# Performance work log

Hardware: AMD Instinct MI355X
Metric: run time of the kernel (lower is better)

Reference implementation:

```python
import jax, jax.numpy as jnp
import numpy as np

N_QUBITS = 4
N_LAYERS = 3
BATCH = 1048576  # 2**20; batched state vector [B, 2,2,2,2] complex64 = 128 MB


def setup_inputs() -> dict:
    key = jax.random.key(0)
    k1, k2 = jax.random.split(key)
    x = jax.random.normal(k1, (BATCH, N_QUBITS), dtype=jnp.float32)
    q_weights = jax.random.normal(k2, (N_LAYERS, N_QUBITS, 3), dtype=jnp.float32) * 0.1
    return {"x": x, "q_weights": q_weights}


def _ry_mat(theta):
    # RY(t) = [[cos t/2, -sin t/2], [sin t/2, cos t/2]]; theta: [] or [B]
    c = jnp.cos(theta * 0.5).astype(jnp.complex64)
    s = jnp.sin(theta * 0.5).astype(jnp.complex64)
    return jnp.stack([jnp.stack([c, -s], -1), jnp.stack([s, c], -1)], -2)


def _rz_mat(theta):
    # RZ(t) = diag(e^{-it/2}, e^{it/2})
    e = jnp.exp(-0.5j * theta.astype(jnp.complex64))
    z = jnp.zeros_like(e)
    return jnp.stack([jnp.stack([e, z], -1), jnp.stack([z, jnp.conj(e)], -1)], -2)


def _apply_1q(state, U, wire):
    # state: [B,2,2,2,2]; U: [2,2] (shared) or [B,2,2] (per-sample)
    ax = wire + 1
    state = jnp.moveaxis(state, ax, -1)
    if U.ndim == 3:
        state = jnp.einsum('b...o,bno->b...n', state, U)
    else:
        state = jnp.einsum('b...o,no->b...n', state, U)
    return jnp.moveaxis(state, -1, ax)


def _cnot(state, c, t):
    # flip target bit on the control=1 slice
    ca, ta = c + 1, t + 1
    s0 = jnp.take(state, 0, axis=ca)
    s1 = jnp.take(state, 1, axis=ca)
    ta2 = ta if ta < ca else ta - 1
    s1 = jnp.flip(s1, axis=ta2)
    return jnp.stack([s0, s1], axis=ca)


def _circuit(x, q_weights):
    B = x.shape[0]
    xn = jnp.tanh(x) * jnp.pi  # [B, 4]
    # |0000>
    state = jnp.zeros((B,) + (2,) * N_QUBITS, dtype=jnp.complex64)
    state = state.at[:, 0, 0, 0, 0].set(1.0 + 0.0j)
    # angle encoding: RY(2x_i) then RZ(x_i), per-sample batched 2x2 gates
    for i in range(N_QUBITS):
        state = _apply_1q(state, _ry_mat(2.0 * xn[:, i]), i)
        state = _apply_1q(state, _rz_mat(xn[:, i]), i)
    # variational layers: Rot(phi,theta,omega) = RZ(omega) @ RY(theta) @ RZ(phi)
    for l in range(N_LAYERS):
        for i in range(N_QUBITS):
            phi, theta, omega = q_weights[l, i, 0], q_weights[l, i, 1], q_weights[l, i, 2]
            U = _rz_mat(omega) @ _ry_mat(theta) @ _rz_mat(phi)
            state = _apply_1q(state, U, i)
        for i in range(N_QUBITS):
            state = _cnot(state, i, (i + 1) % N_QUBITS)
    # <Z_i> = p(bit_i=0) - p(bit_i=1)
    probs = jnp.abs(state) ** 2  # [B,2,2,2,2] real
    evs = []
    for i in range(N_QUBITS):
        axes = tuple(a for a in range(1, N_QUBITS + 1) if a != i + 1)
        marg = jnp.sum(probs, axis=axes)  # [B, 2]
        evs.append(marg[:, 0] - marg[:, 1])
    return jnp.stack(evs, axis=-1).astype(jnp.float32)  # [B, 4]


def reference(x, q_weights):
    return _circuit(x, q_weights)
```

## Files before the change

kernel.cpp:

```cpp
#include <hip/hip_runtime.h>


struct C { float r, i; };

__device__ __forceinline__ C cmul(C a, C b) {
    C o;
    o.r = fmaf(a.r, b.r, -(a.i * b.i));
    o.i = fmaf(a.r, b.i,   a.i * b.r);
    return o;
}

__device__ __forceinline__ C cmadd(float ur, float ui, float wr, float wi, C a, C b) {
    C o;
    o.r = fmaf(ur, a.r, fmaf(-ui, a.i, fmaf(wr, b.r, -(wi * b.i))));
    o.i = fmaf(ur, a.i, fmaf( ui, a.r, fmaf(wr, b.i,   wi * b.r)));
    return o;
}

template <int BP>
__device__ __forceinline__ void apply_gate(C st[16], float4 A4, float4 B4) {
#pragma unroll
    for (int i = 0; i < 8; i++) {
        const int lo = ((i >> BP) << (BP + 1)) | (i & ((1 << BP) - 1));
        const int hi = lo | (1 << BP);
        const C a = st[lo], b = st[hi];
        st[lo] = cmadd(A4.x, A4.y, A4.z, A4.w, a, b);
        st[hi] = cmadd(B4.x, B4.y, B4.z, B4.w, a, b);
    }
}

template <int CB, int TB>
__device__ __forceinline__ void cnot(C st[16]) {
#pragma unroll
    for (int i = 0; i < 16; i++) {
        if ((i & (1 << CB)) && !(i & (1 << TB))) {
            C t = st[i];
            st[i] = st[i | (1 << TB)];
            st[i | (1 << TB)] = t;
        }
    }
}

struct Enc { float r0, i0, r1, i1; };
__device__ __forceinline__ Enc encode(float xq) {
    const float ax = fabsf(xq);
    const float e  = __builtin_amdgcn_exp2f(ax * -2.8853900817779268f);
    const float r  = __builtin_amdgcn_rcpf(1.0f + e);
    const float t  = copysignf((1.0f - e) * r, xq);
    const float sh = __builtin_amdgcn_sinf(t * 0.25f);
    const float ch = __builtin_amdgcn_cosf(t * 0.25f);
    const float s  = 2.0f * sh * ch;
    const float c  = fmaf(-2.0f * sh, sh, 1.0f);
    return {c * ch, -(c * sh), s * ch, s * sh};
}

__global__ __launch_bounds__(256, 6) void qlayer_kernel(const float* __restrict__ x,
                                                        const float* __restrict__ qw,
                                                        float* __restrict__ out, int B) {
    __shared__ float4 Ug[12][2];
    const int tid = threadIdx.x;
    if (tid < 12) {
        const float phi = qw[tid * 3 + 0];
        const float th  = qw[tid * 3 + 1];
        const float om  = qw[tid * 3 + 2];
        float s, c;   __sincosf(0.5f * th, &s, &c);
        float sa, ca; __sincosf(0.5f * (phi + om), &sa, &ca);
        float sb, cb; __sincosf(0.5f * (phi - om), &sb, &cb);
        Ug[tid][0] = make_float4(c * ca, -c * sa, -s * cb, -s * sb);
        Ug[tid][1] = make_float4(s * cb, -s * sb, c * ca, c * sa);
    }
    __syncthreads();

    const int b = blockIdx.x * 256 + tid;
    if (b >= B) return;

    const float4 xv = reinterpret_cast<const float4*>(x)[b];
    const float xs[4] = {xv.x, xv.y, xv.z, xv.w};

    C v[4][2];
#pragma unroll
    for (int q = 0; q < 4; q++) {
        const Enc e = encode(xs[q]);
        const C a{e.r0, e.i0}, bv{e.r1, e.i1};
        const float4 A4 = Ug[q][0], B4 = Ug[q][1];
        v[q][0] = cmadd(A4.x, A4.y, A4.z, A4.w, a, bv);
        v[q][1] = cmadd(B4.x, B4.y, B4.z, B4.w, a, bv);
    }

    C t01[4], t23[4];
#pragma unroll
    for (int i = 0; i < 4; i++) {
        t01[i] = cmul(v[0][(i >> 1) & 1], v[1][i & 1]);
        t23[i] = cmul(v[2][(i >> 1) & 1], v[3][i & 1]);
    }
    C st[16];
#pragma unroll
    for (int i = 0; i < 16; i++) st[i] = cmul(t01[i >> 2], t23[i & 3]);

    cnot<3, 2>(st); cnot<2, 1>(st); cnot<1, 0>(st); cnot<0, 3>(st);

    apply_gate<3>(st, Ug[4][0], Ug[4][1]);
    apply_gate<2>(st, Ug[5][0], Ug[5][1]);
    apply_gate<1>(st, Ug[6][0], Ug[6][1]);
    apply_gate<0>(st, Ug[7][0], Ug[7][1]);
    cnot<3, 2>(st); cnot<2, 1>(st); cnot<1, 0>(st); cnot<0, 3>(st);
    apply_gate<3>(st, Ug[8][0], Ug[8][1]);
    apply_gate<2>(st, Ug[9][0], Ug[9][1]);
    apply_gate<1>(st, Ug[10][0], Ug[10][1]);
    apply_gate<0>(st, Ug[11][0], Ug[11][1]);
    cnot<3, 2>(st); cnot<2, 1>(st); cnot<1, 0>(st); cnot<0, 3>(st);

    float s0 = 0.f, s1 = 0.f, s2 = 0.f, s3 = 0.f;
#pragma unroll
    for (int i = 0; i < 16; i++) {
        const float p = fmaf(st[i].r, st[i].r, st[i].i * st[i].i);
        if (i & 8) s3 += p;
        if (i & 4) s2 += p;
        if (i & 2) s1 += p;
        if (i & 1) s0 += p;
    }

    float4 ev;
    ev.x = fmaf(-2.0f, s3, 1.0f);
    ev.y = fmaf(-2.0f, s2, 1.0f);
    ev.z = fmaf(-2.0f, s1, 1.0f);
    ev.w = fmaf(-2.0f, s0, 1.0f);
    reinterpret_cast<float4*>(out)[b] = ev;
}

extern "C" void kernel_launch(void* const* d_in, const int* in_sizes, int n_in,
                              void* d_out, int out_size, void* d_ws, size_t ws_size,
                              hipStream_t stream) {
    const float* x  = (const float*)d_in[0];
    const float* qw = (const float*)d_in[1];
    float* out = (float*)d_out;
    const int B = in_sizes[0] / 4;
    const int blocks = (B + 255) / 256;
    qlayer_kernel<<<blocks, 256, 0, stream>>>(x, qw, out, B);
}
```

Measured before the change: 97.63 us.

## Precompose variational circuit into 16x16 unitary and apply via split-f16 MFMA

A tiny precompute kernel builds the fixed 16x16 complex unitary of all CNOT and variational layers (layers 1-2) from the weights. It stores it as hi/lo f16 real-embedded 32x32 matrices in workspace. The main kernel writes each sample's state through LDS as split f16 and applies the unitary with three MFMA 16x16x32 products to keep near-fp32 accuracy. This replaces per-thread scalar gate arithmetic with matrix-core work, at the cost of an extra launch, heavy LDS traffic, two block barriers and lower occupancy.

```diff
diff --git a/kernel.cpp b/kernel.cpp
--- a/kernel.cpp
+++ b/kernel.cpp
@@ -1,5 +1,8 @@
 #include <hip/hip_runtime.h>
 
+
+using f16x8 = __attribute__((ext_vector_type(8))) _Float16;
+using f32x4 = __attribute__((ext_vector_type(4))) float;
 
 struct C { float r, i; };
 
@@ -54,9 +57,10 @@
     return {c * ch, -(c * sh), s * ch, s * sh};
 }
 
-__global__ __launch_bounds__(256, 6) void qlayer_kernel(const float* __restrict__ x,
-                                                        const float* __restrict__ qw,
-                                                        float* __restrict__ out, int B) {
+#define WS_WLO 2048
+#define WS_UG0 4096
+
+__global__ void qcompose_kernel(const float* __restrict__ qw, float* __restrict__ ws) {
     __shared__ float4 Ug[12][2];
     const int tid = threadIdx.x;
     if (tid < 12) {
@@ -71,10 +75,74 @@
     }
     __syncthreads();
 
-    const int b = blockIdx.x * 256 + tid;
-    if (b >= B) return;
-
-    const float4 xv = reinterpret_cast<const float4*>(x)[b];
+    if (tid < 4) {
+        float4* o = reinterpret_cast<float4*>(reinterpret_cast<char*>(ws) + WS_UG0);
+        o[2 * tid]     = Ug[tid][0];
+        o[2 * tid + 1] = Ug[tid][1];
+    }
+
+    if (tid < 16) {
+        C st[16];
+#pragma unroll
+        for (int i = 0; i < 16; i++) { st[i].r = 0.0f; st[i].i = 0.0f; }
+        st[tid].r = 1.0f;
+
+        cnot<3, 2>(st); cnot<2, 1>(st); cnot<1, 0>(st); cnot<0, 3>(st);
+        apply_gate<3>(st, Ug[4][0], Ug[4][1]);
+        apply_gate<2>(st, Ug[5][0], Ug[5][1]);
+        apply_gate<1>(st, Ug[6][0], Ug[6][1]);
+        apply_gate<0>(st, Ug[7][0], Ug[7][1]);
+        cnot<3, 2>(st); cnot<2, 1>(st); cnot<1, 0>(st); cnot<0, 3>(st);
+        apply_gate<3>(st, Ug[8][0], Ug[8][1]);
+        apply_gate<2>(st, Ug[9][0], Ug[9][1]);
+        apply_gate<1>(st, Ug[10][0], Ug[10][1]);
+        apply_gate<0>(st, Ug[11][0], Ug[11][1]);
+        cnot<3, 2>(st); cnot<2, 1>(st); cnot<1, 0>(st); cnot<0, 3>(st);
+
+        _Float16* whi = reinterpret_cast<_Float16*>(ws);
+        _Float16* wlo = reinterpret_cast<_Float16*>(reinterpret_cast<char*>(ws) + WS_WLO);
+        const int k0 = 2 * tid, k1 = k0 + 1;
+#pragma unroll
+        for (int d = 0; d < 16; d++) {
+            const int j0 = 2 * d, j1 = j0 + 1;
+            const float vr = st[d].r, vi = st[d].i;
+            float v[4]  = {vr, vi, -vi, vr};
+            int   jj[4] = {j0, j1, j0, j1};
+            int   kk[4] = {k0, k0, k1, k1};
+#pragma unroll
+            for (int e = 0; e < 4; e++) {
+                _Float16 h = (_Float16)v[e];
+                _Float16 l = (_Float16)((v[e] - (float)h) * 2048.0f);
+                whi[jj[e] * 32 + kk[e]] = h;
+                wlo[jj[e] * 32 + kk[e]] = l;
+            }
+        }
+    }
+}
+
+__global__ __launch_bounds__(256, 4) void qlayer_kernel(const float* __restrict__ x,
+                                                        const float* __restrict__ ws,
+                                                        float* __restrict__ out, int B) {
+    __shared__ __align__(16) unsigned char lds[4 * 64 * 144];
+    const int tid  = threadIdx.x;
+    const int lane = tid & 63;
+    const int wid  = tid >> 6;
+    char* slab  = reinterpret_cast<char*>(lds) + wid * (64 * 144);
+    char* myrow = slab + lane * 144;
+
+    const char* wsb = reinterpret_cast<const char*>(ws);
+
+    const int jrow = lane & 15;
+    const int kb   = (lane >> 4) * 16;
+    const f16x8 Bh0 = *reinterpret_cast<const f16x8*>(wsb + jrow * 64 + kb);
+    const f16x8 Bh1 = *reinterpret_cast<const f16x8*>(wsb + (jrow + 16) * 64 + kb);
+    const f16x8 Bl0 = *reinterpret_cast<const f16x8*>(wsb + WS_WLO + jrow * 64 + kb);
+    const f16x8 Bl1 = *reinterpret_cast<const f16x8*>(wsb + WS_WLO + (jrow + 16) * 64 + kb);
+    const float4* ug0 = reinterpret_cast<const float4*>(wsb + WS_UG0);
+
+    const int b  = blockIdx.x * 256 + tid;
+    const int bl = (b < B) ? b : (B - 1);
+    const float4 xv = reinterpret_cast<const float4*>(x)[bl];
     const float xs[4] = {xv.x, xv.y, xv.z, xv.w};
 
     C v[4][2];
@@ -82,7 +150,7 @@
     for (int q = 0; q < 4; q++) {
         const Enc e = encode(xs[q]);
         const C a{e.r0, e.i0}, bv{e.r1, e.i1};
-        const float4 A4 = Ug[q][0], B4 = Ug[q][1];
+        const float4 A4 = ug0[2 * q], B4 = ug0[2 * q + 1];
         v[q][0] = cmadd(A4.x, A4.y, A4.z, A4.w, a, bv);
         v[q][1] = cmadd(B4.x, B4.y, B4.z, B4.w, a, bv);
     }
@@ -97,35 +165,75 @@
 #pragma unroll
     for (int i = 0; i < 16; i++) st[i] = cmul(t01[i >> 2], t23[i & 3]);
 
-    cnot<3, 2>(st); cnot<2, 1>(st); cnot<1, 0>(st); cnot<0, 3>(st);
-
-    apply_gate<3>(st, Ug[4][0], Ug[4][1]);
-    apply_gate<2>(st, Ug[5][0], Ug[5][1]);
-    apply_gate<1>(st, Ug[6][0], Ug[6][1]);
-    apply_gate<0>(st, Ug[7][0], Ug[7][1]);
-    cnot<3, 2>(st); cnot<2, 1>(st); cnot<1, 0>(st); cnot<0, 3>(st);
-    apply_gate<3>(st, Ug[8][0], Ug[8][1]);
-    apply_gate<2>(st, Ug[9][0], Ug[9][1]);
-    apply_gate<1>(st, Ug[10][0], Ug[10][1]);
-    apply_gate<0>(st, Ug[11][0], Ug[11][1]);
-    cnot<3, 2>(st); cnot<2, 1>(st); cnot<1, 0>(st); cnot<0, 3>(st);
+#pragma unroll
+    for (int c = 0; c < 4; c++) {
+        f16x8 vh, vl;
+#pragma unroll
+        for (int d = 0; d < 4; d++) {
+            const float fr = st[4 * c + d].r, fi = st[4 * c + d].i;
+            const _Float16 hr = (_Float16)fr, hi_ = (_Float16)fi;
+            vh[2 * d]     = hr;
+            vh[2 * d + 1] = hi_;
+            vl[2 * d]     = (_Float16)((fr - (float)hr) * 2048.0f);
+            vl[2 * d + 1] = (_Float16)((fi - (float)hi_) * 2048.0f);
+        }
+        *reinterpret_cast<f16x8*>(myrow + c * 16)      = vh;
+        *reinterpret_cast<f16x8*>(myrow + 64 + c * 16) = vl;
+    }
+
+    __syncthreads();
+
+    const f32x4 Z = {0.f, 0.f, 0.f, 0.f};
+#pragma unroll
+    for (int m = 0; m < 4; m++) {
+        const char* arow = slab + (16 * m + (lane & 15)) * 144 + kb;
+        const f16x8 Ah = *reinterpret_cast<const f16x8*>(arow);
+        const f16x8 Al = *reinterpret_cast<const f16x8*>(arow + 64);
+
+        f32x4 main0 = __builtin_amdgcn_mfma_f32_16x16x32_f16(Ah, Bh0, Z, 0, 0, 0);
+        f32x4 corr0 = __builtin_amdgcn_mfma_f32_16x16x32_f16(Ah, Bl0, Z, 0, 0, 0);
+        corr0       = __builtin_amdgcn_mfma_f32_16x16x32_f16(Al, Bh0, corr0, 0, 0, 0);
+        f32x4 main1 = __builtin_amdgcn_mfma_f32_16x16x32_f16(Ah, Bh1, Z, 0, 0, 0);
+        f32x4 corr1 = __builtin_amdgcn_mfma_f32_16x16x32_f16(Ah, Bl1, Z, 0, 0, 0);
+        corr1       = __builtin_amdgcn_mfma_f32_16x16x32_f16(Al, Bh1, corr1, 0, 0, 0);
+
+        const int srow = 16 * m + 4 * (lane >> 4);
+        const int col  = lane & 15;
+#pragma unroll
+        for (int r = 0; r < 4; r++) {
+            float* crow = reinterpret_cast<float*>(slab + (srow + r) * 144);
+            crow[col]      = fmaf(corr0[r], 4.8828125e-4f, main0[r]);
+            crow[16 + col] = fmaf(corr1[r], 4.8828125e-4f, main1[r]);
+        }
+    }
+
+    __syncthreads();
+
+    float cv[32];
+#pragma unroll
+    for (int c = 0; c < 8; c++) {
+        const float4 q4 = *reinterpret_cast<const float4*>(myrow + c * 16);
+        cv[4 * c] = q4.x; cv[4 * c + 1] = q4.y; cv[4 * c + 2] = q4.z; cv[4 * c + 3] = q4.w;
+    }
 
     float s0 = 0.f, s1 = 0.f, s2 = 0.f, s3 = 0.f;
 #pragma unroll
-    for (int i = 0; i < 16; i++) {
-        const float p = fmaf(st[i].r, st[i].r, st[i].i * st[i].i);
-        if (i & 8) s3 += p;
-        if (i & 4) s2 += p;
-        if (i & 2) s1 += p;
-        if (i & 1) s0 += p;
-    }
-
-    float4 ev;
-    ev.x = fmaf(-2.0f, s3, 1.0f);
-    ev.y = fmaf(-2.0f, s2, 1.0f);
-    ev.z = fmaf(-2.0f, s1, 1.0f);
-    ev.w = fmaf(-2.0f, s0, 1.0f);
-    reinterpret_cast<float4*>(out)[b] = ev;
+    for (int d = 0; d < 16; d++) {
+        const float p = fmaf(cv[2 * d], cv[2 * d], cv[2 * d + 1] * cv[2 * d + 1]);
+        if (d & 8) s3 += p;
+        if (d & 4) s2 += p;
+        if (d & 2) s1 += p;
+        if (d & 1) s0 += p;
+    }
+
+    if (b < B) {
+        float4 ev;
+        ev.x = fmaf(-2.0f, s3, 1.0f);
+        ev.y = fmaf(-2.0f, s2, 1.0f);
+        ev.z = fmaf(-2.0f, s1, 1.0f);
+        ev.w = fmaf(-2.0f, s0, 1.0f);
+        reinterpret_cast<float4*>(out)[b] = ev;
+    }
 }
 
 extern "C" void kernel_launch(void* const* d_in, const int* in_sizes, int n_in,
@@ -134,7 +242,9 @@
     const float* x  = (const float*)d_in[0];
     const float* qw = (const float*)d_in[1];
     float* out = (float*)d_out;
+    float* ws  = (float*)d_ws;
     const int B = in_sizes[0] / 4;
     const int blocks = (B + 255) / 256;
-    qlayer_kernel<<<blocks, 256, 0, stream>>>(x, qw, out, B);
-}
+    qcompose_kernel<<<1, 64, 0, stream>>>(qw, ws);
+    qlayer_kernel<<<blocks, 256, 0, stream>>>(x, ws, out, B);
+}
```

After: 84.40 us. 13.6% less time.

## Fold fixed variational circuit into a 16x16 unitary applied via MFMA

Applied to the files above, without the earlier changes.

Precomputes the whole weight-only part of the circuit (CNOTs and variational gates) as a 16x16 complex unitary per block. It stores that unitary in LDS as hi/lo fp16 split matrices and applies it to each sample's fp16-converted product state with 32x32x16 MFMA instructions, replacing the per-thread scalar gate chain. It also switches to a persistent grid-stride loop capped at 1536 blocks, prefetching the next chunk's inputs. The state vector is only carried in fp16, which reduces accuracy, and the design adds LDS traffic, fences and cross-lane shuffles.

```diff
diff --git a/kernel.cpp b/kernel.cpp
--- a/kernel.cpp
+++ b/kernel.cpp
@@ -1,5 +1,8 @@
 #include <hip/hip_runtime.h>
 
+
+using f16x8  = __attribute__((ext_vector_type(8))) _Float16;
+using f32x16 = __attribute__((ext_vector_type(16))) float;
 
 struct C { float r, i; };
 
@@ -54,11 +57,26 @@
     return {c * ch, -(c * sh), s * ch, s * sh};
 }
 
+__device__ __forceinline__ void wave_lds_fence() {
+    asm volatile("s_waitcnt lgkmcnt(0)" ::: "memory");
+    __builtin_amdgcn_sched_barrier(0);
+}
+
+#define ROWB 80
+
 __global__ __launch_bounds__(256, 6) void qlayer_kernel(const float* __restrict__ x,
                                                         const float* __restrict__ qw,
-                                                        float* __restrict__ out, int B) {
+                                                        float* __restrict__ out,
+                                                        int B, int nChunks) {
     __shared__ float4 Ug[12][2];
-    const int tid = threadIdx.x;
+    __shared__ __align__(16) unsigned char Wh_lds[2048];
+    __shared__ __align__(16) unsigned char Wl_lds[2048];
+    __shared__ __align__(16) unsigned char slab_all[4 * 64 * ROWB];
+
+    const int tid  = threadIdx.x;
+    const int lane = tid & 63;
+    const int wid  = tid >> 6;
+
     if (tid < 12) {
         const float phi = qw[tid * 3 + 0];
         const float th  = qw[tid * 3 + 1];
@@ -69,63 +87,149 @@
         Ug[tid][0] = make_float4(c * ca, -c * sa, -s * cb, -s * sb);
         Ug[tid][1] = make_float4(s * cb, -s * sb, c * ca, c * sa);
     }
+    if (tid < 16) {
+        wave_lds_fence();
+        C st[16];
+#pragma unroll
+        for (int i = 0; i < 16; i++) { st[i].r = 0.0f; st[i].i = 0.0f; }
+        st[tid].r = 1.0f;
+
+        cnot<3, 2>(st); cnot<2, 1>(st); cnot<1, 0>(st); cnot<0, 3>(st);
+        apply_gate<3>(st, Ug[4][0], Ug[4][1]);
+        apply_gate<2>(st, Ug[5][0], Ug[5][1]);
+        apply_gate<1>(st, Ug[6][0], Ug[6][1]);
+        apply_gate<0>(st, Ug[7][0], Ug[7][1]);
+        cnot<3, 2>(st); cnot<2, 1>(st); cnot<1, 0>(st); cnot<0, 3>(st);
+        apply_gate<3>(st, Ug[8][0], Ug[8][1]);
+        apply_gate<2>(st, Ug[9][0], Ug[9][1]);
+        apply_gate<1>(st, Ug[10][0], Ug[10][1]);
+        apply_gate<0>(st, Ug[11][0], Ug[11][1]);
+        cnot<3, 2>(st); cnot<2, 1>(st); cnot<1, 0>(st); cnot<0, 3>(st);
+
+        unsigned* whiW = reinterpret_cast<unsigned*>(Wh_lds);
+        unsigned* wloW = reinterpret_cast<unsigned*>(Wl_lds);
+#pragma unroll
+        for (int d = 0; d < 16; d++) {
+            const float vr = st[d].r, vi = st[d].i;
+            const _Float16 hr  = (_Float16)vr, hi_ = (_Float16)vi;
+            const _Float16 lr  = (_Float16)((vr - (float)hr)  * 2048.0f);
+            const _Float16 li  = (_Float16)((vi - (float)hi_) * 2048.0f);
+            const unsigned uhr = (unsigned)__builtin_bit_cast(unsigned short, hr);
+            const unsigned uhi = (unsigned)__builtin_bit_cast(unsigned short, hi_);
+            const unsigned ulr = (unsigned)__builtin_bit_cast(unsigned short, lr);
+            const unsigned uli = (unsigned)__builtin_bit_cast(unsigned short, li);
+            whiW[(2 * d) * 16 + tid]     = uhr | ((uhi ^ 0x8000u) << 16);
+            whiW[(2 * d + 1) * 16 + tid] = uhi | (uhr << 16);
+            wloW[(2 * d) * 16 + tid]     = ulr | ((uli ^ 0x8000u) << 16);
+            wloW[(2 * d + 1) * 16 + tid] = uli | (ulr << 16);
+        }
+    }
     __syncthreads();
 
-    const int b = blockIdx.x * 256 + tid;
-    if (b >= B) return;
-
-    const float4 xv = reinterpret_cast<const float4*>(x)[b];
-    const float xs[4] = {xv.x, xv.y, xv.z, xv.w};
-
-    C v[4][2];
-#pragma unroll
-    for (int q = 0; q < 4; q++) {
-        const Enc e = encode(xs[q]);
-        const C a{e.r0, e.i0}, bv{e.r1, e.i1};
-        const float4 A4 = Ug[q][0], B4 = Ug[q][1];
-        v[q][0] = cmadd(A4.x, A4.y, A4.z, A4.w, a, bv);
-        v[q][1] = cmadd(B4.x, B4.y, B4.z, B4.w, a, bv);
-    }
-
-    C t01[4], t23[4];
-#pragma unroll
-    for (int i = 0; i < 4; i++) {
-        t01[i] = cmul(v[0][(i >> 1) & 1], v[1][i & 1]);
-        t23[i] = cmul(v[2][(i >> 1) & 1], v[3][i & 1]);
-    }
-    C st[16];
-#pragma unroll
-    for (int i = 0; i < 16; i++) st[i] = cmul(t01[i >> 2], t23[i & 3]);
-
-    cnot<3, 2>(st); cnot<2, 1>(st); cnot<1, 0>(st); cnot<0, 3>(st);
-
-    apply_gate<3>(st, Ug[4][0], Ug[4][1]);
-    apply_gate<2>(st, Ug[5][0], Ug[5][1]);
-    apply_gate<1>(st, Ug[6][0], Ug[6][1]);
-    apply_gate<0>(st, Ug[7][0], Ug[7][1]);
-    cnot<3, 2>(st); cnot<2, 1>(st); cnot<1, 0>(st); cnot<0, 3>(st);
-    apply_gate<3>(st, Ug[8][0], Ug[8][1]);
-    apply_gate<2>(st, Ug[9][0], Ug[9][1]);
-    apply_gate<1>(st, Ug[10][0], Ug[10][1]);
-    apply_gate<0>(st, Ug[11][0], Ug[11][1]);
-    cnot<3, 2>(st); cnot<2, 1>(st); cnot<1, 0>(st); cnot<0, 3>(st);
-
-    float s0 = 0.f, s1 = 0.f, s2 = 0.f, s3 = 0.f;
-#pragma unroll
-    for (int i = 0; i < 16; i++) {
-        const float p = fmaf(st[i].r, st[i].r, st[i].i * st[i].i);
-        if (i & 8) s3 += p;
-        if (i & 4) s2 += p;
-        if (i & 2) s1 += p;
-        if (i & 1) s0 += p;
-    }
-
-    float4 ev;
-    ev.x = fmaf(-2.0f, s3, 1.0f);
-    ev.y = fmaf(-2.0f, s2, 1.0f);
-    ev.z = fmaf(-2.0f, s1, 1.0f);
-    ev.w = fmaf(-2.0f, s0, 1.0f);
-    reinterpret_cast<float4*>(out)[b] = ev;
+    const int j32 = lane & 31;
+    const int h   = lane >> 5;
+    const f16x8 Wh0 = *reinterpret_cast<const f16x8*>(Wh_lds + j32 * 64 + h * 16);
+    const f16x8 Wh1 = *reinterpret_cast<const f16x8*>(Wh_lds + j32 * 64 + 32 + h * 16);
+    const f16x8 Wl0 = *reinterpret_cast<const f16x8*>(Wl_lds + j32 * 64 + h * 16);
+    const f16x8 Wl1 = *reinterpret_cast<const f16x8*>(Wl_lds + j32 * 64 + 32 + h * 16);
+
+    char* slab  = reinterpret_cast<char*>(slab_all) + wid * (64 * ROWB);
+    char* myrow = slab + lane * ROWB;
+    const float4* x4 = reinterpret_cast<const float4*>(x);
+
+    int chunk = blockIdx.x;
+    if (chunk >= nChunks) return;
+    int b = chunk * 256 + tid;
+    float4 xv = x4[b < B ? b : (B - 1)];
+
+    while (true) {
+        const float xs[4] = {xv.x, xv.y, xv.z, xv.w};
+
+        C v[4][2];
+#pragma unroll
+        for (int q = 0; q < 4; q++) {
+            const Enc e = encode(xs[q]);
+            const C a{e.r0, e.i0}, bv{e.r1, e.i1};
+            const float4 A4 = Ug[q][0], B4 = Ug[q][1];
+            v[q][0] = cmadd(A4.x, A4.y, A4.z, A4.w, a, bv);
+            v[q][1] = cmadd(B4.x, B4.y, B4.z, B4.w, a, bv);
+        }
+
+        C t01[4], t23[4];
+#pragma unroll
+        for (int i = 0; i < 4; i++) {
+            t01[i] = cmul(v[0][(i >> 1) & 1], v[1][i & 1]);
+            t23[i] = cmul(v[2][(i >> 1) & 1], v[3][i & 1]);
+        }
+        f16x8 vh[4];
+#pragma unroll
+        for (int i = 0; i < 16; i++) {
+            const C s = cmul(t01[i >> 2], t23[i & 3]);
+            vh[i >> 2][2 * (i & 3)]     = (_Float16)s.r;
+            vh[i >> 2][2 * (i & 3) + 1] = (_Float16)s.i;
+        }
+        wave_lds_fence();
+#pragma unroll
+        for (int c = 0; c < 4; c++)
+            *reinterpret_cast<f16x8*>(myrow + c * 16) = vh[c];
+
+        const int nextChunk = chunk + gridDim.x;
+        const bool more = nextChunk < nChunks;
+        int bn = 0; float4 xn;
+        if (more) {
+            bn = nextChunk * 256 + tid;
+            xn = x4[bn < B ? bn : (B - 1)];
+        }
+
+        wave_lds_fence();
+
+        float r3[2], r2[2], r1[2], r0[2];
+#pragma unroll
+        for (int n = 0; n < 2; n++) {
+            const char* srow = slab + (32 * n + j32) * ROWB + h * 16;
+            const f16x8 S0 = *reinterpret_cast<const f16x8*>(srow);
+            const f16x8 S1 = *reinterpret_cast<const f16x8*>(srow + 32);
+            const f32x16 Z = {0.f,0.f,0.f,0.f,0.f,0.f,0.f,0.f,
+                              0.f,0.f,0.f,0.f,0.f,0.f,0.f,0.f};
+            f32x16 D = __builtin_amdgcn_mfma_f32_32x32x16_f16(Wh0, S0, Z, 0, 0, 0);
+            D        = __builtin_amdgcn_mfma_f32_32x32x16_f16(Wh1, S1, D, 0, 0, 0);
+            f32x16 L = __builtin_amdgcn_mfma_f32_32x32x16_f16(Wl0, S0, Z, 0, 0, 0);
+            L        = __builtin_amdgcn_mfma_f32_32x32x16_f16(Wl1, S1, L, 0, 0, 0);
+
+            float p[8];
+#pragma unroll
+            for (int m = 0; m < 8; m++) {
+                const float c0 = fmaf(L[2 * m],     4.8828125e-4f, D[2 * m]);
+                const float c1 = fmaf(L[2 * m + 1], 4.8828125e-4f, D[2 * m + 1]);
+                p[m] = fmaf(c1, c1, c0 * c0);
+            }
+            const float e67 = p[6] + p[7];
+            float t3 = (p[4] + p[5]) + e67;
+            float t2 = (p[2] + p[3]) + e67;
+            float t0 = (p[1] + p[3]) + (p[5] + p[7]);
+            const float tAll = ((p[0] + p[2]) + (p[4] + p[6])) + t0;
+            float t1 = h ? tAll : 0.0f;
+            t3 += __shfl_xor(t3, 32); t2 += __shfl_xor(t2, 32);
+            t1 += __shfl_xor(t1, 32); t0 += __shfl_xor(t0, 32);
+            r3[n] = t3; r2[n] = t2; r1[n] = t1; r0[n] = t0;
+        }
+        const float e3 = h ? r3[1] : r3[0];
+        const float e2 = h ? r2[1] : r2[0];
+        const float e1 = h ? r1[1] : r1[0];
+        const float e0 = h ? r0[1] : r0[0];
+
+        if (b < B) {
+            float4 ev;
+            ev.x = fmaf(-2.0f, e3, 1.0f);
+            ev.y = fmaf(-2.0f, e2, 1.0f);
+            ev.z = fmaf(-2.0f, e1, 1.0f);
+            ev.w = fmaf(-2.0f, e0, 1.0f);
+            reinterpret_cast<float4*>(out)[b] = ev;
+        }
+
+        if (!more) break;
+        chunk = nextChunk; b = bn; xv = xn;
+    }
 }
 
 extern "C" void kernel_launch(void* const* d_in, const int* in_sizes, int n_in,
@@ -135,6 +239,7 @@
     const float* qw = (const float*)d_in[1];
     float* out = (float*)d_out;
     const int B = in_sizes[0] / 4;
-    const int blocks = (B + 255) / 256;
-    qlayer_kernel<<<blocks, 256, 0, stream>>>(x, qw, out, B);
-}
+    const int nChunks = (B + 255) / 256;
+    const int grid = nChunks < 1536 ? nChunks : 1536;
+    qlayer_kernel<<<grid, 256, 0, stream>>>(x, qw, out, B, nChunks);
+}
```

Measured after the change: 122.4 us. +25.3%, slower.
